# Performance work log

Hardware: AMD Instinct MI355X
Metric: run time of the kernel (lower is better)

Reference implementation:

```python
import jax, jax.numpy as jnp
import numpy as np

B, T, C, H, S = 8, 2048, 1024, 16, 64
EPS = 1e-5


def layernorm(x, g, b):
    m = jnp.mean(x, axis=-1, keepdims=True)
    v = jnp.mean((x - m) ** 2, axis=-1, keepdims=True)
    return (x - m) * jax.lax.rsqrt(v + EPS) * g + b


def wkv6(r, k, v, time_decay, u):
    # r,k,v: [B,T,H,S]; time_decay,u: [H,S]
    # kernel receives ew=-exp(w) and uses decay = exp(ew) = exp(-exp(w))
    d = jnp.exp(-jnp.exp(time_decay))  # [H,S], in (0,1)

    def step(state, rkv):
        r_t, k_t, v_t = rkv  # each [B,H,S]
        kv = k_t[..., :, None] * v_t[..., None, :]  # [B,H,S,S] outer product
        y = jnp.einsum('bhk,bhkv->bhv', r_t, state + u[None, :, :, None] * kv)
        state = state * d[None, :, :, None] + kv
        return state, y

    s0 = jnp.zeros((B, H, S, S), r.dtype)
    rkv_tm = (jnp.moveaxis(r, 1, 0), jnp.moveaxis(k, 1, 0), jnp.moveaxis(v, 1, 0))
    _, ys = jax.lax.scan(step, s0, rkv_tm)  # ys: [T,B,H,S]
    return jnp.moveaxis(ys, 0, 1).reshape(B, T, C)


def setup_inputs() -> dict:
    key = jax.random.key(0)
    ks = jax.random.split(key, 10)
    sc = C ** -0.5
    return {
        'x': jax.random.normal(ks[0], (B, T, C), jnp.float32),
        'time_decay': -5.0 + 0.5 * jax.random.normal(ks[1], (H, S), jnp.float32),
        'time_first': 0.1 * jax.random.normal(ks[2], (H, S), jnp.float32),
        'w_r': sc * jax.random.normal(ks[3], (C, C), jnp.float32),
        'w_k': sc * jax.random.normal(ks[4], (C, C), jnp.float32),
        'w_v': sc * jax.random.normal(ks[5], (C, C), jnp.float32),
        'w_o': sc * jax.random.normal(ks[6], (C, C), jnp.float32),
        'w_fk': sc * jax.random.normal(ks[7], (C, 4 * C), jnp.float32),
        'w_fv': (4 * C) ** -0.5 * jax.random.normal(ks[8], (4 * C, C), jnp.float32),
        'g1': jnp.ones((C,), jnp.float32),
        'b1': jnp.zeros((C,), jnp.float32),
        'g2': jnp.ones((C,), jnp.float32),
        'b2': jnp.zeros((C,), jnp.float32),
    }


def reference(x, time_decay, time_first, w_r, w_k, w_v, w_o, w_fk, w_fv, g1, b1, g2, b2):
    x_ln = layernorm(x, g1, b1)
    r = (x_ln @ w_r).reshape(B, T, H, S)
    k = (x_ln @ w_k).reshape(B, T, H, S)
    v = (x_ln @ w_v).reshape(B, T, H, S)
    wkv = wkv6(r, k, v, time_decay, time_first)  # [B,T,C]
    rwkv = jax.nn.sigmoid(r.reshape(B, T, C)) * wkv
    x = x + rwkv @ w_o
    x_ln2 = layernorm(x, g2, b2)
    ffn = (jax.nn.relu(x_ln2 @ w_fk) ** 2) @ w_fv
    return x + ffn
```

## Files before the change

### kernel.cpp

```cpp
#include <hip/hip_runtime.h>
#include <hip/hip_bf16.h>

#define B_ 8
#define T_ 2048
#define C_ 1024
#define H_ 16
#define S_ 64
#define BT_ (B_*T_)
#define FF_ (4*C_)
#define NC_ 32

typedef __attribute__((ext_vector_type(8))) short short8;
typedef __attribute__((ext_vector_type(4))) float f32x4;

union U8 { uint4 v; unsigned short s[8]; };

static __device__ __forceinline__ unsigned short f2bf(float f){
  unsigned u = __float_as_uint(f);
  unsigned r = (u + 0x7fffu + ((u >> 16) & 1u)) >> 16;
  return (unsigned short)r;
}
static __device__ __forceinline__ float bf2f(unsigned short u){
  return __uint_as_float(((unsigned)u) << 16);
}

static __device__ __forceinline__ void gll16(const unsigned short* g, unsigned short* l){
  __builtin_amdgcn_global_load_lds((const __attribute__((address_space(1))) void*)g,
                                   (__attribute__((address_space(3))) void*)l, 16, 0, 0);
}

__global__ __launch_bounds__(256) void ln_kernel(const float* __restrict__ x,
    const float* __restrict__ g, const float* __restrict__ b,
    unsigned short* __restrict__ out){
  int row = blockIdx.x;
  int tid = threadIdx.x;
  const float4* xr = reinterpret_cast<const float4*>(x + (size_t)row * C_);
  float4 v = xr[tid];
  float s = v.x + v.y + v.z + v.w;
  float q = v.x*v.x + v.y*v.y + v.z*v.z + v.w*v.w;
  int lane = tid & 63, w = tid >> 6;
  #pragma unroll
  for (int off = 32; off; off >>= 1){ s += __shfl_down(s, off); q += __shfl_down(q, off); }
  __shared__ float red[2][4];
  if (lane == 0){ red[0][w] = s; red[1][w] = q; }
  __syncthreads();
  s = red[0][0] + red[0][1] + red[0][2] + red[0][3];
  q = red[1][0] + red[1][1] + red[1][2] + red[1][3];
  float mean = s * (1.0f / C_);
  float var  = q * (1.0f / C_) - mean * mean;
  float inv = rsqrtf(var + 1e-5f);
  float4 gg = reinterpret_cast<const float4*>(g)[tid];
  float4 bb = reinterpret_cast<const float4*>(b)[tid];
  ushort4 o;
  o.x = f2bf((v.x - mean) * inv * gg.x + bb.x);
  o.y = f2bf((v.y - mean) * inv * gg.y + bb.y);
  o.z = f2bf((v.z - mean) * inv * gg.z + bb.z);
  o.w = f2bf((v.w - mean) * inv * gg.w + bb.w);
  reinterpret_cast<ushort4*>(out + (size_t)row * C_)[tid] = o;
}

__global__ __launch_bounds__(256) void wconv_kernel(const float* __restrict__ w,
    unsigned short* __restrict__ wt, int K, int N){
  __shared__ float tile[32][33];
  int bk = blockIdx.x * 32, bn = blockIdx.y * 32;
  int tx = threadIdx.x & 31, ty = threadIdx.x >> 5;
  #pragma unroll
  for (int i = 0; i < 4; i++)
    tile[ty + 8*i][tx] = w[(size_t)(bk + ty + 8*i) * N + bn + tx];
  __syncthreads();
  #pragma unroll
  for (int i = 0; i < 4; i++)
    wt[(size_t)(bn + ty + 8*i) * K + bk + tx] = f2bf(tile[tx][ty + 8*i]);
}

#define EPI_RKV 1
#define EPI_WO  2
#define EPI_FK  3
#define EPI_FV  4

template<int EPI>
__global__ __launch_bounds__(256, 2) void gemm_kernel(
    const unsigned short* __restrict__ A,
    const unsigned short* __restrict__ Bt,
    void* __restrict__ outp,
    const float* __restrict__ aux,
    int K, int nx){
  __shared__ unsigned short As[2][128][32];
  __shared__ unsigned short Bs[2][128][32];
  const int tid = threadIdx.x;

  int nwg = gridDim.x;
  int id  = blockIdx.x;
  id = (id & 7) * (nwg >> 3) + (id >> 3);
  int gsz = nx << 2;
  int g = id / gsz, rem = id % gsz;
  const int bm = ((g << 2) + (rem & 3)) * 128;
  const int bn = (rem >> 2) * 128;

  const int lane = tid & 63, wv = tid >> 6;
  const int wm = wv >> 1, wn = wv & 1;
  const int ml = lane & 15, klo = (lane >> 4) * 8;

  const int srow = wv * 16 + (lane >> 2);
  const int scol = (lane & 3) * 8;
  const unsigned short* Ag0 = A  + (size_t)(bm + srow) * K + scol;
  const unsigned short* Ag1 = Ag0 + (size_t)64 * K;
  const unsigned short* Bg0 = Bt + (size_t)(bn + srow) * K + scol;
  const unsigned short* Bg1 = Bg0 + (size_t)64 * K;

  f32x4 acc[4][4];
  #pragma unroll
  for (int i = 0; i < 4; i++)
    #pragma unroll
    for (int j = 0; j < 4; j++)
      acc[i][j] = (f32x4){0.f, 0.f, 0.f, 0.f};

  const int NT = K >> 5;
  auto stage = [&](int p, int kt){
    size_t ko = (size_t)kt * 32;
    gll16(Ag0 + ko, &As[p][wv*16][0]);
    gll16(Ag1 + ko, &As[p][64 + wv*16][0]);
    gll16(Bg0 + ko, &Bs[p][wv*16][0]);
    gll16(Bg1 + ko, &Bs[p][64 + wv*16][0]);
  };

  stage(0, 0);
  __syncthreads();
  for (int kt = 0; kt < NT; ++kt){
    const int p = kt & 1;
    if (kt + 1 < NT) stage(p ^ 1, kt + 1);
    short8 af[4], bfv[4];
    #pragma unroll
    for (int mf = 0; mf < 4; mf++)
      af[mf] = *reinterpret_cast<const short8*>(&As[p][wm*64 + mf*16 + ml][klo]);
    #pragma unroll
    for (int nf = 0; nf < 4; nf++)
      bfv[nf] = *reinterpret_cast<const short8*>(&Bs[p][wn*64 + nf*16 + ml][klo]);
    #pragma unroll
    for (int mf = 0; mf < 4; mf++)
      #pragma unroll
      for (int nf = 0; nf < 4; nf++)
        acc[mf][nf] = __builtin_amdgcn_mfma_f32_16x16x32_bf16(af[mf], bfv[nf], acc[mf][nf], 0, 0, 0);
    __syncthreads();
  }

  const int rbase = bm + wm*64 + (lane >> 4) * 4;
  const int cbase = bn + wn*64 + ml;
  #pragma unroll
  for (int mf = 0; mf < 4; mf++){
    #pragma unroll
    for (int nf = 0; nf < 4; nf++){
      #pragma unroll
      for (int r = 0; r < 4; r++){
        int m = rbase + mf*16 + r;
        int n = cbase + nf*16;
        float vv = acc[mf][nf][r];
        if (EPI == EPI_RKV){
          unsigned short* o = (unsigned short*)outp;
          int b = m >> 11, t = m & (T_ - 1);
          int h = n >> 6,  s = n & (S_ - 1);
          o[(((size_t)(b * H_ + h)) * T_ + t) * S_ + s] = f2bf(vv);
        } else if (EPI == EPI_WO){
          float* o = (float*)outp;
          o[(size_t)m * C_ + n] = aux[(size_t)m * C_ + n] + vv;
        } else if (EPI == EPI_FK){
          unsigned short* o = (unsigned short*)outp;
          float rl = vv > 0.f ? vv : 0.f;
          o[(size_t)m * FF_ + n] = f2bf(rl * rl);
        } else {
          float* o = (float*)outp;
          o[(size_t)m * C_ + n] += vv;
        }
      }
    }
  }
}


__global__ __launch_bounds__(256) void wkv_p1(
    const unsigned short* __restrict__ kT, const unsigned short* __restrict__ vT,
    const float* __restrict__ td, unsigned short* __restrict__ AS){
  const int bid = blockIdx.x;
  const int bh = bid >> 5, c = bid & (NC_ - 1);
  const int h = bh & (H_ - 1);
  const int tid = threadIdx.x, lane = tid & 63, w = tid >> 6;
  __shared__ unsigned short kh[64][72];
  __shared__ unsigned short vt[64][72];
  __shared__ float eps[64];
  if (tid < 64) eps[tid] = expf(td[h * S_ + tid]);
  __syncthreads();
  const int t = tid >> 2, q = (tid & 3) * 16;
  const size_t base = ((size_t)bh * T_ + c * 64 + t) * S_ + q;
  U8 k0, k1, v0, v1;
  k0.v = *(const uint4*)(kT + base);  k1.v = *(const uint4*)(kT + base + 8);
  v0.v = *(const uint4*)(vT + base);  v1.v = *(const uint4*)(vT + base + 8);
  const float mt = -(float)(63 - t);
  #pragma unroll
  for (int j = 0; j < 8; j++){
    int k = q + j;
    kh[k][t] = f2bf(bf2f(k0.s[j]) * expf(mt * eps[k]));
    vt[k][t] = v0.s[j];
  }
  #pragma unroll
  for (int j = 0; j < 8; j++){
    int k = q + 8 + j;
    kh[k][t] = f2bf(bf2f(k1.s[j]) * expf(mt * eps[k]));
    vt[k][t] = v1.s[j];
  }
  __syncthreads();
  const int ml = lane & 15, klo = (lane >> 4) * 8;
  f32x4 acc[4];
  #pragma unroll
  for (int nf = 0; nf < 4; nf++) acc[nf] = (f32x4){0.f,0.f,0.f,0.f};
  #pragma unroll
  for (int ks = 0; ks < 2; ks++){
    short8 af = *(const short8*)&vt[w*16 + ml][ks*32 + klo];
    #pragma unroll
    for (int nf = 0; nf < 4; nf++){
      short8 bfr = *(const short8*)&kh[nf*16 + ml][ks*32 + klo];
      acc[nf] = __builtin_amdgcn_mfma_f32_16x16x32_bf16(af, bfr, acc[nf], 0, 0, 0);
    }
  }
  unsigned short* dst = AS + ((size_t)bid * 64 + w*16 + (lane >> 4) * 4) * 64;
  #pragma unroll
  for (int nf = 0; nf < 4; nf++)
    #pragma unroll
    for (int r = 0; r < 4; r++)
      dst[(size_t)r * 64 + nf*16 + ml] = f2bf(acc[nf][r]);
}

__global__ __launch_bounds__(256) void wkv_p2(
    unsigned short* __restrict__ AS, const float* __restrict__ td){
  const int bh = blockIdx.x >> 2, vs = blockIdx.x & 3;
  const int h = bh & (H_ - 1);
  const int tid = threadIdx.x;
  const int vo = tid >> 4, k4 = (tid & 15) * 4;
  const int v = vs * 16 + vo;
  float dL[4], S[4];
  #pragma unroll
  for (int j = 0; j < 4; j++){
    dL[j] = expf(-64.f * expf(td[h * S_ + k4 + j]));
    S[j] = 0.f;
  }
  const size_t rb = ((size_t)bh * NC_ * 64 + v) * 64 + k4;
  for (int c = 0; c < NC_; c++){
    unsigned short* p = AS + rb + (size_t)c * 4096;
    ushort4 A = *(const ushort4*)p;
    ushort4 o;
    o.x = f2bf(S[0]); o.y = f2bf(S[1]); o.z = f2bf(S[2]); o.w = f2bf(S[3]);
    *(ushort4*)p = o;
    S[0] = fmaf(S[0], dL[0], bf2f(A.x)); S[1] = fmaf(S[1], dL[1], bf2f(A.y));
    S[2] = fmaf(S[2], dL[2], bf2f(A.z)); S[3] = fmaf(S[3], dL[3], bf2f(A.w));
  }
}

__global__ __launch_bounds__(256) void wkv_p3(
    const unsigned short* __restrict__ rT, const unsigned short* __restrict__ kT,
    const unsigned short* __restrict__ vT, const unsigned short* __restrict__ Sb,
    const float* __restrict__ td, const float* __restrict__ tf,
    unsigned short* __restrict__ rwkv){
  const int bid = blockIdx.x;
  const int bh = bid >> 5, c = bid & (NC_ - 1);
  const int b = bh >> 4, h = bh & (H_ - 1);
  const int tid = threadIdx.x, lane = tid & 63, w = tid >> 6;
  __shared__ unsigned short Rt[64][72];
  __shared__ unsigned short Kt[64][72];
  __shared__ unsigned short Vt[64][72];
  __shared__ unsigned short Sc[64][72];
  __shared__ float eps[64], us[64], diag[64];
  __shared__ float dred[64][4];

  if (tid < 64){ eps[tid] = expf(td[h * S_ + tid]); us[tid] = tf[h * S_ + tid]; }
  __syncthreads();

  const int t = tid >> 2, q = (tid & 3) * 16;
  const size_t base  = ((size_t)bh * T_ + c * 64 + t) * S_ + q;
  const size_t sbase = (((size_t)bh * NC_ + c) * 64 + t) * 64 + q;
  {
    U8 r0, r1, k0, k1, v0, v1, s0, s1, rt0, rt1, kt0, kt1;
    r0.v = *(const uint4*)(rT + base);  r1.v = *(const uint4*)(rT + base + 8);
    k0.v = *(const uint4*)(kT + base);  k1.v = *(const uint4*)(kT + base + 8);
    v0.v = *(const uint4*)(vT + base);  v1.v = *(const uint4*)(vT + base + 8);
    s0.v = *(const uint4*)(Sb + sbase); s1.v = *(const uint4*)(Sb + sbase + 8);
    float dpart = 0.f;
    const float ft = (float)t;
    #pragma unroll
    for (int j = 0; j < 8; j++){
      int k = q + j;
      float ep = eps[k];
      float rv = bf2f(r0.s[j]), kv = bf2f(k0.s[j]);
      rt0.s[j] = f2bf(rv * expf(-ft * ep));
      kt0.s[j] = f2bf(kv * expf((ft + 1.f) * ep));
      dpart = fmaf(rv * us[k], kv, dpart);
      Vt[k][t] = v0.s[j];
    }
    #pragma unroll
    for (int j = 0; j < 8; j++){
      int k = q + 8 + j;
      float ep = eps[k];
      float rv = bf2f(r1.s[j]), kv = bf2f(k1.s[j]);
      rt1.s[j] = f2bf(rv * expf(-ft * ep));
      kt1.s[j] = f2bf(kv * expf((ft + 1.f) * ep));
      dpart = fmaf(rv * us[k], kv, dpart);
      Vt[k][t] = v1.s[j];
    }
    *(uint4*)&Rt[t][q]     = rt0.v;  *(uint4*)&Rt[t][q + 8] = rt1.v;
    *(uint4*)&Kt[t][q]     = kt0.v;  *(uint4*)&Kt[t][q + 8] = kt1.v;
    *(uint4*)&Sc[t][q]     = s0.v;   *(uint4*)&Sc[t][q + 8] = s1.v;
    dred[t][tid & 3] = dpart;
  }
  __syncthreads();
  if (tid < 64) diag[tid] = dred[tid][0] + dred[tid][1] + dred[tid][2] + dred[tid][3];

  const int ml = lane & 15, klo = (lane >> 4) * 8;
  f32x4 acc1[4];
  #pragma unroll
  for (int nf = 0; nf < 4; nf++) acc1[nf] = (f32x4){0.f,0.f,0.f,0.f};
  #pragma unroll
  for (int ks = 0; ks < 2; ks++){
    short8 af = *(const short8*)&Rt[w*16 + ml][ks*32 + klo];
    #pragma unroll
    for (int nf = 0; nf < 4; nf++){
      short8 bfr = *(const short8*)&Kt[nf*16 + ml][ks*32 + klo];
      acc1[nf] = __builtin_amdgcn_mfma_f32_16x16x32_bf16(af, bfr, acc1[nf], 0, 0, 0);
    }
  }
  __syncthreads();

  #pragma unroll
  for (int nf = 0; nf < 4; nf++){
    #pragma unroll
    for (int r = 0; r < 4; r++){
      int tt = w*16 + (lane >> 4) * 4 + r;
      int ii = nf*16 + ml;
      float e = acc1[nf][r];
      float val = (ii < tt) ? e : (ii == tt ? diag[tt] : 0.f);
      Kt[tt][ii] = f2bf(val);
    }
  }
  __syncthreads();

  f32x4 acc2[4];
  #pragma unroll
  for (int nf = 0; nf < 4; nf++) acc2[nf] = (f32x4){0.f,0.f,0.f,0.f};
  #pragma unroll
  for (int ks = 0; ks < 2; ks++){
    short8 aA = *(const short8*)&Kt[w*16 + ml][ks*32 + klo];
    short8 aR = *(const short8*)&Rt[w*16 + ml][ks*32 + klo];
    #pragma unroll
    for (int nf = 0; nf < 4; nf++){
      short8 bV = *(const short8*)&Vt[nf*16 + ml][ks*32 + klo];
      acc2[nf] = __builtin_amdgcn_mfma_f32_16x16x32_bf16(aA, bV, acc2[nf], 0, 0, 0);
      short8 bS = *(const short8*)&Sc[nf*16 + ml][ks*32 + klo];
      acc2[nf] = __builtin_amdgcn_mfma_f32_16x16x32_bf16(aR, bS, acc2[nf], 0, 0, 0);
    }
  }

  const size_t rrow = ((size_t)bh * T_ + c * 64) * S_;
  #pragma unroll
  for (int nf = 0; nf < 4; nf++){
    #pragma unroll
    for (int r = 0; r < 4; r++){
      int tt = w*16 + (lane >> 4) * 4 + r;
      int vv = nf*16 + ml;
      float y = acc2[nf][r];
      float rv = bf2f(rT[rrow + (size_t)tt * S_ + vv]);
      float sig = 1.f / (1.f + expf(-rv));
      rwkv[((size_t)b * T_ + c * 64 + tt) * C_ + h * S_ + vv] = f2bf(sig * y);
    }
  }
}

extern "C" void kernel_launch(void* const* d_in, const int* in_sizes, int n_in,
                              void* d_out, int out_size, void* d_ws, size_t ws_size,
                              hipStream_t stream){
  const float* x    = (const float*)d_in[0];
  const float* td   = (const float*)d_in[1];
  const float* tf   = (const float*)d_in[2];
  const float* w_r  = (const float*)d_in[3];
  const float* w_k  = (const float*)d_in[4];
  const float* w_v  = (const float*)d_in[5];
  const float* w_o  = (const float*)d_in[6];
  const float* w_fk = (const float*)d_in[7];
  const float* w_fv = (const float*)d_in[8];
  const float* g1   = (const float*)d_in[9];
  const float* b1   = (const float*)d_in[10];
  const float* g2   = (const float*)d_in[11];
  const float* b2   = (const float*)d_in[12];
  float* out = (float*)d_out;

  char* ws = (char*)d_ws;
  size_t off = 0;
  auto alloc = [&](size_t bytes){ char* p = ws + off; off += (bytes + 255) & ~(size_t)255; return p; };
  unsigned short* wrT  = (unsigned short*)alloc((size_t)C_ * C_ * 2);
  unsigned short* wkT  = (unsigned short*)alloc((size_t)C_ * C_ * 2);
  unsigned short* wvT  = (unsigned short*)alloc((size_t)C_ * C_ * 2);
  unsigned short* woT  = (unsigned short*)alloc((size_t)C_ * C_ * 2);
  unsigned short* wfkT = (unsigned short*)alloc((size_t)C_ * FF_ * 2);
  unsigned short* wfvT = (unsigned short*)alloc((size_t)FF_ * C_ * 2);
  unsigned short* xln  = (unsigned short*)alloc((size_t)BT_ * C_ * 2);
  unsigned short* rT   = (unsigned short*)alloc((size_t)BT_ * C_ * 2);
  unsigned short* kT   = (unsigned short*)alloc((size_t)BT_ * C_ * 2);
  unsigned short* vT   = (unsigned short*)alloc((size_t)BT_ * C_ * 2);
  unsigned short* rwkv = (unsigned short*)alloc((size_t)BT_ * C_ * 2);
  unsigned short* hbuf = rT;
  unsigned short* AS   = xln;

  dim3 blk(256);

  wconv_kernel<<<dim3(C_/32,  C_/32),  blk, 0, stream>>>(w_r,  wrT,  C_,  C_);
  wconv_kernel<<<dim3(C_/32,  C_/32),  blk, 0, stream>>>(w_k,  wkT,  C_,  C_);
  wconv_kernel<<<dim3(C_/32,  C_/32),  blk, 0, stream>>>(w_v,  wvT,  C_,  C_);
  wconv_kernel<<<dim3(C_/32,  C_/32),  blk, 0, stream>>>(w_o,  woT,  C_,  C_);
  wconv_kernel<<<dim3(C_/32,  FF_/32), blk, 0, stream>>>(w_fk, wfkT, C_,  FF_);
  wconv_kernel<<<dim3(FF_/32, C_/32),  blk, 0, stream>>>(w_fv, wfvT, FF_, C_);

  ln_kernel<<<BT_, blk, 0, stream>>>(x, g1, b1, xln);

  gemm_kernel<EPI_RKV><<<dim3((C_/128)*(BT_/128)), blk, 0, stream>>>(xln, wrT, rT, nullptr, C_, C_/128);
  gemm_kernel<EPI_RKV><<<dim3((C_/128)*(BT_/128)), blk, 0, stream>>>(xln, wkT, kT, nullptr, C_, C_/128);
  gemm_kernel<EPI_RKV><<<dim3((C_/128)*(BT_/128)), blk, 0, stream>>>(xln, wvT, vT, nullptr, C_, C_/128);

  wkv_p1<<<B_*H_*NC_, blk, 0, stream>>>(kT, vT, td, AS);
  wkv_p2<<<B_*H_*4,   blk, 0, stream>>>(AS, td);
  wkv_p3<<<B_*H_*NC_, blk, 0, stream>>>(rT, kT, vT, AS, td, tf, rwkv);

  gemm_kernel<EPI_WO><<<dim3((C_/128)*(BT_/128)), blk, 0, stream>>>(rwkv, woT, out, x, C_, C_/128);

  ln_kernel<<<BT_, blk, 0, stream>>>(out, g2, b2, xln);

  gemm_kernel<EPI_FK><<<dim3((FF_/128)*(BT_/128)), blk, 0, stream>>>(xln, wfkT, hbuf, nullptr, C_, FF_/128);
  gemm_kernel<EPI_FV><<<dim3((C_/128)*(BT_/128)), blk, 0, stream>>>(hbuf, wfvT, out, nullptr, FF_, C_/128);
}
```

Measured before the change: 648.4 us.

## Switch GEMMs to 256x256 tiles with triple-buffered LDS, swizzle, and fused RKV launch

Replaces the 128x128, 256-thread GEMM with a 256x256, 512-thread kernel. It uses a three-stage LDS pipeline with explicit vmcnt waits and barriers, an XOR swizzle on LDS columns to avoid bank conflicts, and raised wave priority (s_setprio) around the MFMA block. The three r/k/v projections run as one launch over contiguous weight buffers, and the output index selects which buffer to write. The larger tiles improve operand reuse and cut launch count, but use 96 KB of LDS and more accumulator registers per thread, so occupancy may drop. The fused launch depends on wrT/wkT/wvT and rT/kT/vT being contiguous in the workspace, which holds because each size is a multiple of 256 bytes.

```diff
diff --git a/kernel.cpp b/kernel.cpp
--- a/kernel.cpp
+++ b/kernel.cpp
@@ -73,20 +73,20 @@
     wt[(size_t)(bn + ty + 8*i) * K + bk + tx] = f2bf(tile[tx][ty + 8*i]);
 }
 
-#define EPI_RKV 1
-#define EPI_WO  2
-#define EPI_FK  3
-#define EPI_FV  4
+#define EPI_RKV3 1
+#define EPI_WO   2
+#define EPI_FK   3
+#define EPI_FV   4
 
 template<int EPI>
-__global__ __launch_bounds__(256, 2) void gemm_kernel(
+__global__ __launch_bounds__(512, 2) void gemm256_kernel(
     const unsigned short* __restrict__ A,
     const unsigned short* __restrict__ Bt,
     void* __restrict__ outp,
     const float* __restrict__ aux,
     int K, int nx){
-  __shared__ unsigned short As[2][128][32];
-  __shared__ unsigned short Bs[2][128][32];
+  __shared__ unsigned short As[3][256][32];
+  __shared__ unsigned short Bs[3][256][32];
   const int tid = threadIdx.x;
 
   int nwg = gridDim.x;
@@ -94,60 +94,76 @@
   id = (id & 7) * (nwg >> 3) + (id >> 3);
   int gsz = nx << 2;
   int g = id / gsz, rem = id % gsz;
-  const int bm = ((g << 2) + (rem & 3)) * 128;
-  const int bn = (rem >> 2) * 128;
-
-  const int lane = tid & 63, wv = tid >> 6;
-  const int wm = wv >> 1, wn = wv & 1;
-  const int ml = lane & 15, klo = (lane >> 4) * 8;
-
-  const int srow = wv * 16 + (lane >> 2);
-  const int scol = (lane & 3) * 8;
-  const unsigned short* Ag0 = A  + (size_t)(bm + srow) * K + scol;
-  const unsigned short* Ag1 = Ag0 + (size_t)64 * K;
-  const unsigned short* Bg0 = Bt + (size_t)(bn + srow) * K + scol;
-  const unsigned short* Bg1 = Bg0 + (size_t)64 * K;
-
-  f32x4 acc[4][4];
-  #pragma unroll
-  for (int i = 0; i < 4; i++)
+  const int bm = ((g << 2) + (rem & 3)) * 256;
+  const int bn = (rem >> 2) * 256;
+
+  const int lane = tid & 63, wid = tid >> 6;
+  const int wr = wid >> 2, wc = wid & 3;
+  const int ml = lane & 15, hi = lane >> 4;
+  const int scol = ((hi ^ (ml & 3)) << 3);
+
+  const int sr  = (lane >> 2);
+  const int ssl = (lane & 3) ^ (sr & 3);
+  const unsigned short* aP0 = A  + (size_t)(bm + wid*16 + sr) * K + ssl*8;
+  const unsigned short* aP1 = aP0 + (size_t)128 * K;
+  const unsigned short* bP0 = Bt + (size_t)(bn + wid*16 + sr) * K + ssl*8;
+  const unsigned short* bP1 = bP0 + (size_t)128 * K;
+
+  f32x4 acc[8][4];
+  #pragma unroll
+  for (int i = 0; i < 8; i++)
     #pragma unroll
     for (int j = 0; j < 4; j++)
       acc[i][j] = (f32x4){0.f, 0.f, 0.f, 0.f};
 
   const int NT = K >> 5;
-  auto stage = [&](int p, int kt){
+  auto stage = [&](int bf, int kt){
     size_t ko = (size_t)kt * 32;
-    gll16(Ag0 + ko, &As[p][wv*16][0]);
-    gll16(Ag1 + ko, &As[p][64 + wv*16][0]);
-    gll16(Bg0 + ko, &Bs[p][wv*16][0]);
-    gll16(Bg1 + ko, &Bs[p][64 + wv*16][0]);
+    gll16(aP0 + ko, &As[bf][wid*16][0]);
+    gll16(aP1 + ko, &As[bf][128 + wid*16][0]);
+    gll16(bP0 + ko, &Bs[bf][wid*16][0]);
+    gll16(bP1 + ko, &Bs[bf][128 + wid*16][0]);
   };
-
-  stage(0, 0);
-  __syncthreads();
-  for (int kt = 0; kt < NT; ++kt){
-    const int p = kt & 1;
-    if (kt + 1 < NT) stage(p ^ 1, kt + 1);
-    short8 af[4], bfv[4];
-    #pragma unroll
-    for (int mf = 0; mf < 4; mf++)
-      af[mf] = *reinterpret_cast<const short8*>(&As[p][wm*64 + mf*16 + ml][klo]);
+  auto compute = [&](int bf){
+    short8 bvr[4];
     #pragma unroll
     for (int nf = 0; nf < 4; nf++)
-      bfv[nf] = *reinterpret_cast<const short8*>(&Bs[p][wn*64 + nf*16 + ml][klo]);
-    #pragma unroll
-    for (int mf = 0; mf < 4; mf++)
+      bvr[nf] = *(const short8*)&Bs[bf][wc*64 + nf*16 + ml][scol];
+    __builtin_amdgcn_s_setprio(1);
+    #pragma unroll
+    for (int mf = 0; mf < 8; mf++){
+      short8 af = *(const short8*)&As[bf][wr*128 + mf*16 + ml][scol];
       #pragma unroll
       for (int nf = 0; nf < 4; nf++)
-        acc[mf][nf] = __builtin_amdgcn_mfma_f32_16x16x32_bf16(af[mf], bfv[nf], acc[mf][nf], 0, 0, 0);
-    __syncthreads();
-  }
-
-  const int rbase = bm + wm*64 + (lane >> 4) * 4;
-  const int cbase = bn + wn*64 + ml;
-  #pragma unroll
-  for (int mf = 0; mf < 4; mf++){
+        acc[mf][nf] = __builtin_amdgcn_mfma_f32_16x16x32_bf16(af, bvr[nf], acc[mf][nf], 0, 0, 0);
+    }
+    __builtin_amdgcn_s_setprio(0);
+  };
+
+  stage(0, 0);
+  stage(1, 1);
+  int bf = 0;
+  for (int kt = 0; kt < NT - 2; ++kt){
+    int b2 = bf + 2; if (b2 >= 3) b2 -= 3;
+    stage(b2, kt + 2);
+    asm volatile("s_waitcnt vmcnt(8)" ::: "memory");
+    asm volatile("s_barrier" ::: "memory");
+    compute(bf);
+    asm volatile("s_barrier" ::: "memory");
+    bf = bf + 1; if (bf >= 3) bf -= 3;
+  }
+  asm volatile("s_waitcnt vmcnt(4)" ::: "memory");
+  asm volatile("s_barrier" ::: "memory");
+  compute(bf);
+  bf = bf + 1; if (bf >= 3) bf -= 3;
+  asm volatile("s_waitcnt vmcnt(0)" ::: "memory");
+  asm volatile("s_barrier" ::: "memory");
+  compute(bf);
+
+  const int rbase = bm + wr*128 + hi*4;
+  const int cbase = bn + wc*64 + ml;
+  #pragma unroll
+  for (int mf = 0; mf < 8; mf++){
     #pragma unroll
     for (int nf = 0; nf < 4; nf++){
       #pragma unroll
@@ -155,11 +171,11 @@
         int m = rbase + mf*16 + r;
         int n = cbase + nf*16;
         float vv = acc[mf][nf][r];
-        if (EPI == EPI_RKV){
+        if (EPI == EPI_RKV3){
           unsigned short* o = (unsigned short*)outp;
           int b = m >> 11, t = m & (T_ - 1);
-          int h = n >> 6,  s = n & (S_ - 1);
-          o[(((size_t)(b * H_ + h)) * T_ + t) * S_ + s] = f2bf(vv);
+          int which = n >> 10, h = (n >> 6) & (H_ - 1), s = n & (S_ - 1);
+          o[(size_t)which * BT_ * C_ + (((size_t)(b * H_ + h)) * T_ + t) * S_ + s] = f2bf(vv);
         } else if (EPI == EPI_WO){
           float* o = (float*)outp;
           o[(size_t)m * C_ + n] = aux[(size_t)m * C_ + n] + vv;
@@ -407,6 +423,7 @@
   unsigned short* AS   = xln;
 
   dim3 blk(256);
+  dim3 blk5(512);
 
   wconv_kernel<<<dim3(C_/32,  C_/32),  blk, 0, stream>>>(w_r,  wrT,  C_,  C_);
   wconv_kernel<<<dim3(C_/32,  C_/32),  blk, 0, stream>>>(w_k,  wkT,  C_,  C_);
@@ -417,18 +434,16 @@
 
   ln_kernel<<<BT_, blk, 0, stream>>>(x, g1, b1, xln);
 
-  gemm_kernel<EPI_RKV><<<dim3((C_/128)*(BT_/128)), blk, 0, stream>>>(xln, wrT, rT, nullptr, C_, C_/128);
-  gemm_kernel<EPI_RKV><<<dim3((C_/128)*(BT_/128)), blk, 0, stream>>>(xln, wkT, kT, nullptr, C_, C_/128);
-  gemm_kernel<EPI_RKV><<<dim3((C_/128)*(BT_/128)), blk, 0, stream>>>(xln, wvT, vT, nullptr, C_, C_/128);
+  gemm256_kernel<EPI_RKV3><<<dim3((3*C_/256)*(BT_/256)), blk5, 0, stream>>>(xln, wrT, rT, nullptr, C_, 3*C_/256);
 
   wkv_p1<<<B_*H_*NC_, blk, 0, stream>>>(kT, vT, td, AS);
   wkv_p2<<<B_*H_*4,   blk, 0, stream>>>(AS, td);
   wkv_p3<<<B_*H_*NC_, blk, 0, stream>>>(rT, kT, vT, AS, td, tf, rwkv);
 
-  gemm_kernel<EPI_WO><<<dim3((C_/128)*(BT_/128)), blk, 0, stream>>>(rwkv, woT, out, x, C_, C_/128);
+  gemm256_kernel<EPI_WO><<<dim3((C_/256)*(BT_/256)), blk5, 0, stream>>>(rwkv, woT, out, x, C_, C_/256);
 
   ln_kernel<<<BT_, blk, 0, stream>>>(out, g2, b2, xln);
 
-  gemm_kernel<EPI_FK><<<dim3((FF_/128)*(BT_/128)), blk, 0, stream>>>(xln, wfkT, hbuf, nullptr, C_, FF_/128);
-  gemm_kernel<EPI_FV><<<dim3((C_/128)*(BT_/128)), blk, 0, stream>>>(hbuf, wfvT, out, nullptr, FF_, C_/128);
-}
+  gemm256_kernel<EPI_FK><<<dim3((FF_/256)*(BT_/256)), blk5, 0, stream>>>(xln, wfkT, hbuf, nullptr, C_, FF_/256);
+  gemm256_kernel<EPI_FV><<<dim3((C_/256)*(BT_/256)), blk5, 0, stream>>>(hbuf, wfvT, out, nullptr, FF_, C_/256);
+}
```

After: 716.5 us. 1.11x slower.
